# Performance work log

Measured on AMD Instinct MI355X. Metric: run time of the kernel, lower is better.

## Reference

```python
import jax, jax.numpy as jnp
import numpy as np

H = 1024
B = 8
S = 2048

def setup_inputs() -> dict:
    key = jax.random.key(0)
    ks = jax.random.split(key, 16)
    w = lambda k, shp: (jax.random.normal(k, shp, dtype=jnp.float32) * 0.02)
    return {
        "hidden_states": jax.random.normal(ks[0], (B, S, H), dtype=jnp.float32),
        "context_vector": jax.random.normal(ks[1], (B, H), dtype=jnp.float32),
        # nn.Linear weights stored torch-style as [out, in]
        "Wq": w(ks[2], (H, H)), "bq": w(ks[3], (H,)),
        "Wk": w(ks[4], (H, H)), "bk": w(ks[5], (H,)),
        "Wv": w(ks[6], (H, H)), "bv": w(ks[7], (H,)),
        "Wcq": w(ks[8], (H, H)),  # only .weight.t() used in original (no bias)
        "Wck": w(ks[9], (H, H)),
        "g_qh": jax.random.normal(ks[10], (H, 1), dtype=jnp.float32),
        "g_kh": jax.random.normal(ks[11], (H, 1), dtype=jnp.float32),
        "g_qc": jax.random.normal(ks[12], (H, 1), dtype=jnp.float32),
        "g_kc": jax.random.normal(ks[13], (H, 1), dtype=jnp.float32),
    }

def reference(hidden_states, context_vector, Wq, bq, Wk, bk, Wv, bv, Wcq, Wck, g_qh, g_kh, g_qc, g_kc):
    # Linear projections (torch Linear: x @ W.T + b)
    query = jnp.einsum('bsh,oh->bso', hidden_states, Wq) + bq   # [B,S,H]
    key_  = jnp.einsum('bsh,oh->bso', hidden_states, Wk) + bk
    value = jnp.einsum('bsh,oh->bso', hidden_states, Wv) + bv

    # gate = sigmoid(Q @ g_h + (ctx @ g_c)[:,None,:])  -> [B,S,1]
    q_gate = jax.nn.sigmoid(query @ g_qh + (context_vector @ g_qc)[:, None, :])
    k_gate = jax.nn.sigmoid(key_  @ g_kh + (context_vector @ g_kc)[:, None, :])

    # context projections: ctx @ weight.t() (no bias in original usage) -> [B,1,H]
    ctx_q = (context_vector @ Wcq.T)[:, None, :]
    ctx_k = (context_vector @ Wck.T)[:, None, :]

    query_hat = (1.0 - q_gate) * query + q_gate * ctx_q
    key_hat   = (1.0 - k_gate) * key_  + k_gate * ctx_k

    scale = 1.0 / jnp.sqrt(jnp.asarray(H, dtype=jnp.float32))
    scores = jnp.einsum('bqh,bkh->bqk', query_hat, key_hat) * scale  # [B,S,S]
    probs = jax.nn.softmax(scores, axis=-1)
    output = jnp.einsum('bqk,bkh->bqh', probs, value)  # [B,S,H]
    return (output, scores)
```

## Files before the change

kernel.cpp:

```cpp
#include <hip/hip_runtime.h>
#include <cstdint>
#include <cstddef>

#define H 1024
#define NB 8
#define S 2048
#define MROWS (NB*S)

using short8  = __attribute__((ext_vector_type(8))) short;
using ushort8 = __attribute__((ext_vector_type(8))) unsigned short;
using f32x4   = __attribute__((ext_vector_type(4))) float;

__device__ __forceinline__ unsigned short f2bf(float f){
  union { float f; unsigned int u; } c; c.f = f;
  unsigned int u = c.u;
  return (unsigned short)((u + 0x7fffu + ((u >> 16) & 1u)) >> 16);
}
__device__ __forceinline__ float bf2f(unsigned short b){
  union { unsigned int u; float f; } c; c.u = ((unsigned int)b) << 16;
  return c.f;
}

__global__ __launch_bounds__(256) void k_prep(
    const float* __restrict__ Wq, const float* __restrict__ Wk, const float* __restrict__ Wv,
    const float* __restrict__ Wcq, const float* __restrict__ Wck, const float* __restrict__ ctx,
    const float* __restrict__ gqh, const float* __restrict__ gkh,
    const float* __restrict__ bq, const float* __restrict__ bk,
    const float* __restrict__ gqc, const float* __restrict__ gkc,
    unsigned short* __restrict__ wqb, unsigned short* __restrict__ wkb, unsigned short* __restrict__ wvb,
    float* __restrict__ up, float* __restrict__ ctxq, float* __restrict__ ctxk,
    float* __restrict__ scal)
{
  __shared__ float cs[NB * H];
  const int bid = blockIdx.x;
  const int t = threadIdx.x;
  if (bid < 3072){
    const int y = bid >> 10;
    const int x = bid & 1023;
    const float* src = y == 0 ? Wq : (y == 1 ? Wk : Wv);
    unsigned short* dst = y == 0 ? wqb : (y == 1 ? wkb : wvb);
    const int i = (x * 256 + t) * 4;
    float4 v = *reinterpret_cast<const float4*>(src + i);
    ushort4 o; o.x = f2bf(v.x); o.y = f2bf(v.y); o.z = f2bf(v.z); o.w = f2bf(v.w);
    *reinterpret_cast<ushort4*>(dst + i) = o;
  } else if (bid < 3136){
    const int sub = bid - 3072;
    const int z = sub >> 5;
    const int y = (sub >> 2) & 7;
    const int x = sub & 3;
    const float* W = z ? Wk : Wq;
    const float* g = z ? gkh : gqh;
    const int in = x * 256 + t;
    const int o0 = y * 128;
    float s = 0.f;
    for (int o = 0; o < 128; ++o) s = fmaf(W[(size_t)(o0 + o) * H + in], g[o0 + o], s);
    up[(z * 8 + y) * 1024 + in] = s;
  } else if (bid < 3648){
    const int sub = bid - 3136;
    const int y = sub >> 8;
    const int x = sub & 255;
    const float* W = y ? Wck : Wcq;
    float* out = y ? ctxk : ctxq;
    for (int i = t; i < NB * H; i += 256) cs[i] = ctx[i];
    __syncthreads();
    const int wid = t >> 6, lane = t & 63;
    const int row = x * 4 + wid;
    float a[NB];
    #pragma unroll
    for (int b = 0; b < NB; ++b) a[b] = 0.f;
    for (int i0 = 0; i0 < H; i0 += 64){
      const float w = W[(size_t)row * H + i0 + lane];
      #pragma unroll
      for (int b = 0; b < NB; ++b) a[b] = fmaf(w, cs[b * H + i0 + lane], a[b]);
    }
    #pragma unroll
    for (int b = 0; b < NB; ++b){
      float v = a[b];
      #pragma unroll
      for (int off = 32; off > 0; off >>= 1) v += __shfl_xor(v, off);
      if (lane == 0) out[b * H + row] = v;
    }
  } else {
    const int wid = t >> 6, lane = t & 63;
    for (int d = wid; d < 18; d += 4){
      const float *pa, *pb;
      if (d == 0){ pa = bq; pb = gqh; }
      else if (d == 1){ pa = bk; pb = gkh; }
      else if (d < 10){ pa = ctx + (d - 2) * H; pb = gqc; }
      else { pa = ctx + (d - 10) * H; pb = gkc; }
      float s = 0.f;
      for (int i = lane; i < H; i += 64) s = fmaf(pa[i], pb[i], s);
      #pragma unroll
      for (int off = 32; off > 0; off >>= 1) s += __shfl_xor(s, off);
      if (lane == 0) scal[d] = s;
    }
  }
}

__global__ void k_ucombine(const float* __restrict__ up, float* __restrict__ u2){
  int i = blockIdx.x * 256 + threadIdx.x;
  int z = i >> 10, h = i & 1023;
  float s = 0.f;
  #pragma unroll
  for (int c = 0; c < 8; ++c) s += up[(z * 8 + c) * 1024 + h];
  u2[i] = s;
}

__global__ __launch_bounds__(256) void k_prepass(const float* __restrict__ hs,
    const float* __restrict__ u2, const float* __restrict__ scal,
    unsigned short* __restrict__ hsb, float* __restrict__ gq, float* __restrict__ gk){
  const int t = threadIdx.x, wid = t >> 6, lane = t & 63;
  const int row = blockIdx.x * 4 + wid;
  const float* hrow = hs + (size_t)row * H;
  const float* u_q = u2;
  const float* u_k = u2 + 1024;
  unsigned short* orow = hsb + (size_t)row * H;
  float sq = 0.f, sk = 0.f;
  #pragma unroll
  for (int c = 0; c < 4; ++c){
    const int idx = (lane + c * 64) * 4;
    float4 v  = *reinterpret_cast<const float4*>(hrow + idx);
    float4 uq = *reinterpret_cast<const float4*>(u_q + idx);
    float4 uk = *reinterpret_cast<const float4*>(u_k + idx);
    ushort4 o; o.x = f2bf(v.x); o.y = f2bf(v.y); o.z = f2bf(v.z); o.w = f2bf(v.w);
    *reinterpret_cast<ushort4*>(orow + idx) = o;
    sq += v.x*uq.x + v.y*uq.y + v.z*uq.z + v.w*uq.w;
    sk += v.x*uk.x + v.y*uk.y + v.z*uk.z + v.w*uk.w;
  }
  #pragma unroll
  for (int off = 32; off > 0; off >>= 1){
    sq += __shfl_xor(sq, off);
    sk += __shfl_xor(sk, off);
  }
  if (lane == 0){
    const int b = row >> 11;
    gq[row] = 1.f / (1.f + __expf(-(sq + scal[0] + scal[2 + b])));
    gk[row] = 1.f / (1.f + __expf(-(sk + scal[1] + scal[10 + b])));
  }
}


#define VM0() do { asm volatile("s_waitcnt vmcnt(0)" ::: "memory"); } while(0)
#define BAR() do { asm volatile("" ::: "memory"); __builtin_amdgcn_s_barrier(); asm volatile("" ::: "memory"); } while(0)

template<int MODE>
__global__ __launch_bounds__(256, 3)
void k_gemm(const unsigned short* __restrict__ A, const unsigned short* __restrict__ B,
            int K, int ldA, int ldB, long long Abatch, long long Bbatch,
            const float* __restrict__ gq, const float* __restrict__ gk,
            const float* __restrict__ bq, const float* __restrict__ bk, const float* __restrict__ bv,
            const float* __restrict__ cq, const float* __restrict__ ck,
            unsigned short* __restrict__ oq, unsigned short* __restrict__ ok, unsigned short* __restrict__ ov,
            float* __restrict__ outf, long long outBatch, float scale, float* __restrict__ rsum)
{
  __shared__ __align__(16) short lds[20480];
  short* As = lds;
  short* Bs = lds + 8192;

  const int t = threadIdx.x;
  const int wid = t >> 6, lane = t & 63;
  const int wr = wid >> 1, wc = wid & 1;
  const int bz = blockIdx.z;
  const unsigned short* Ab = A + (size_t)bz * (size_t)Abatch;
  const unsigned short* Bb = B + (size_t)bz * (size_t)Bbatch;
  const int row0 = blockIdx.x * 128;
  const int col0 = blockIdx.y * 128;

  const unsigned short* srcA[4];
  const unsigned short* srcB[4];
  #pragma unroll
  for (int i = 0; i < 4; ++i){
    const int c = (wid*4 + i)*64 + lane;
    const int r = c >> 3, sl = c & 7;
    const int kcg = sl ^ (r & 7);
    srcA[i] = Ab + (size_t)(row0 + r) * (size_t)ldA + kcg*8;
    srcB[i] = Bb + (size_t)(col0 + r) * (size_t)ldB + kcg*8;
  }

  f32x4 acc[4][4] = {};
  short8 af[4], bf[4];

  const int nkt = K >> 6;
  for (int kt = 0; kt < nkt; ++kt){
    const int k0 = kt << 6;
    #pragma unroll
    for (int i = 0; i < 4; ++i){
      __builtin_amdgcn_global_load_lds(
        (const __attribute__((address_space(1))) void*)(srcA[i] + k0),
        (__attribute__((address_space(3))) void*)((char*)As + (wid*4 + i)*1024), 16, 0, 0);
      __builtin_amdgcn_global_load_lds(
        (const __attribute__((address_space(1))) void*)(srcB[i] + k0),
        (__attribute__((address_space(3))) void*)((char*)Bs + (wid*4 + i)*1024), 16, 0, 0);
    }
    VM0(); BAR();
    #pragma unroll
    for (int kk = 0; kk < 2; ++kk){
      #pragma unroll
      for (int m = 0; m < 4; ++m){
        const int ar = wr*64 + m*16 + (lane & 15);
        const int ssl = (kk*4 + (lane >> 4)) ^ (ar & 7);
        af[m] = *reinterpret_cast<const short8*>(&As[ar*64 + ssl*8]);
      }
      #pragma unroll
      for (int n = 0; n < 4; ++n){
        const int br = wc*64 + n*16 + (lane & 15);
        const int ssl = (kk*4 + (lane >> 4)) ^ (br & 7);
        bf[n] = *reinterpret_cast<const short8*>(&Bs[br*64 + ssl*8]);
      }
      __builtin_amdgcn_s_setprio(1);
      #pragma unroll
      for (int m = 0; m < 4; ++m)
        #pragma unroll
        for (int n = 0; n < 4; ++n)
          acc[m][n] = __builtin_amdgcn_mfma_f32_16x16x32_bf16(af[m], bf[n], acc[m][n], 0, 0, 0);
      __builtin_amdgcn_s_setprio(0);
    }
    BAR();
  }

  if constexpr (MODE == 0){
    const int which = col0 >> 10;
    const int lcol  = col0 & 1023;
    if (which < 2){
      const float* gate = which ? gk : gq;
      const float* bias = which ? bk : bq;
      const float* ctxv = which ? ck : cq;
      unsigned short* outb = which ? ok : oq;
      unsigned short* tp = (unsigned short*)lds;
      float* gl = (float*)((char*)lds + 34816);
      float* bl = gl + 128;
      float* cl = bl + 128;
      const int b = row0 >> 11;
      __syncthreads();
      if (t < 128){
        gl[t] = gate[row0 + t];
        bl[t] = bias[lcol + t];
        cl[t] = ctxv[b * H + lcol + t];
      }
      __syncthreads();
      #pragma unroll
      for (int m = 0; m < 4; ++m)
        #pragma unroll
        for (int r = 0; r < 4; ++r){
          const int lr = wr*64 + m*16 + (lane >> 4)*4 + r;
          const float g = gl[lr];
          #pragma unroll
          for (int n = 0; n < 4; ++n){
            const int lc = wc*64 + n*16 + (lane & 15);
            const float q = acc[m][n][r] + bl[lc];
            tp[lr*136 + lc] = f2bf((1.f - g) * q + g * cl[lc]);
          }
        }
      __syncthreads();
      const int rr = t & 127;
      const int cc = (t >> 7) * 64;
      const unsigned short* srcp = tp + rr*136 + cc;
      unsigned short* dst = outb + (size_t)(row0 + rr) * H + lcol + cc;
      #pragma unroll
      for (int i = 0; i < 64; i += 8)
        *reinterpret_cast<ushort8*>(dst + i) = *reinterpret_cast<const ushort8*>(srcp + i);
    } else {
      unsigned short* tp = (unsigned short*)lds;
      const int bb = row0 >> 11;
      const int s0 = row0 & (S - 1);
      __syncthreads();
      #pragma unroll
      for (int m = 0; m < 4; ++m)
        #pragma unroll
        for (int r = 0; r < 4; ++r){
          const int lr = wr*64 + m*16 + (lane >> 4)*4 + r;
          #pragma unroll
          for (int n = 0; n < 4; ++n){
            const int lc = wc*64 + n*16 + (lane & 15);
            tp[lc*136 + lr] = f2bf(acc[m][n][r] + bv[lcol + lc]);
          }
        }
      __syncthreads();
      const int hh = t & 127;
      const int sc = (t >> 7) * 64;
      const unsigned short* srcp = tp + hh*136 + sc;
      unsigned short* vout = ov + (size_t)bb * H * S + (size_t)(lcol + hh) * S + (size_t)(s0 + sc);
      #pragma unroll
      for (int i = 0; i < 64; i += 8)
        *reinterpret_cast<ushort8*>(vout + i) = *reinterpret_cast<const ushort8*>(srcp + i);
    }
  } else if constexpr (MODE == 3){
    float* rowacc = (float*)lds;
    __syncthreads();
    if (t < 128) rowacc[t] = 0.f;
    __syncthreads();
    #pragma unroll
    for (int m = 0; m < 4; ++m)
      #pragma unroll
      for (int r = 0; r < 4; ++r){
        const int lr = wr*64 + m*16 + (lane >> 4)*4 + r;
        const int grow = row0 + lr;
        float psum = 0.f;
        #pragma unroll
        for (int n = 0; n < 4; ++n){
          const int gcol = col0 + wc*64 + n*16 + (lane & 15);
          const float val = acc[m][n][r] * scale;
          outf[(size_t)bz * (size_t)outBatch + (size_t)grow * S + gcol] = val;
          const float pe = __expf(fminf(val, 80.f));
          const unsigned short pb = f2bf(pe);
          oq[(size_t)bz * (size_t)outBatch + (size_t)grow * S + gcol] = pb;
          psum += bf2f(pb);
        }
        #pragma unroll
        for (int off = 1; off < 16; off <<= 1) psum += __shfl_xor(psum, off);
        if ((lane & 15) == 0) atomicAdd(&rowacc[lr], psum);
      }
    __syncthreads();
    if (t < 128) atomicAdd(&rsum[bz * S + row0 + t], rowacc[t]);
  } else {
    float* rs = (float*)lds;
    __syncthreads();
    if (t < 128) rs[t] = 1.f / fmaxf(rsum[bz * S + row0 + t], 1e-35f);
    __syncthreads();
    #pragma unroll
    for (int m = 0; m < 4; ++m)
      #pragma unroll
      for (int r = 0; r < 4; ++r){
        const int lr = wr*64 + m*16 + (lane >> 4)*4 + r;
        const float inv = rs[lr];
        #pragma unroll
        for (int n = 0; n < 4; ++n){
          const int gcol = col0 + wc*64 + n*16 + (lane & 15);
          outf[(size_t)bz * (size_t)outBatch + (size_t)(row0 + lr) * H + gcol] = acc[m][n][r] * inv;
        }
      }
  }
}

extern "C" void kernel_launch(void* const* d_in, const int* in_sizes, int n_in,
                              void* d_out, int out_size, void* d_ws, size_t ws_size,
                              hipStream_t stream) {
  const float* hs  = (const float*)d_in[0];
  const float* ctx = (const float*)d_in[1];
  const float* Wq  = (const float*)d_in[2];
  const float* bq  = (const float*)d_in[3];
  const float* Wk  = (const float*)d_in[4];
  const float* bk  = (const float*)d_in[5];
  const float* Wv  = (const float*)d_in[6];
  const float* bv  = (const float*)d_in[7];
  const float* Wcq = (const float*)d_in[8];
  const float* Wck = (const float*)d_in[9];
  const float* gqh = (const float*)d_in[10];
  const float* gkh = (const float*)d_in[11];
  const float* gqc = (const float*)d_in[12];
  const float* gkc = (const float*)d_in[13];

  char* ws = (char*)d_ws;
  unsigned short* hsb   = (unsigned short*)(ws);
  unsigned short* qhat  = (unsigned short*)(ws + 33554432);
  unsigned short* khat  = (unsigned short*)(ws + 67108864);
  unsigned short* vt    = (unsigned short*)(ws + 100663296);
  unsigned short* probs = (unsigned short*)(ws + 134217728);
  unsigned short* wqb   = (unsigned short*)(ws + 201326592);
  unsigned short* wkb   = (unsigned short*)(ws + 203423744);
  unsigned short* wvb   = (unsigned short*)(ws + 205520896);
  float* up    = (float*)(ws + 207618048);
  float* u2    = (float*)(ws + 207683584);
  float* ctxq  = (float*)(ws + 207691776);
  float* ctxk  = (float*)(ws + 207724544);
  float* gq    = (float*)(ws + 207757312);
  float* gk    = (float*)(ws + 207822848);
  float* scal  = (float*)(ws + 207888384);
  float* rsum  = (float*)(ws + 207888640);

  float* out_attn   = (float*)d_out;
  float* out_scores = out_attn + (size_t)MROWS * H;

  hipMemsetAsync(rsum, 0, MROWS * sizeof(float), stream);

  k_prep<<<3649, 256, 0, stream>>>(Wq, Wk, Wv, Wcq, Wck, ctx, gqh, gkh, bq, bk, gqc, gkc,
      wqb, wkb, wvb, up, ctxq, ctxk, scal);
  k_ucombine<<<8, 256, 0, stream>>>(up, u2);
  k_prepass<<<MROWS / 4, 256, 0, stream>>>(hs, u2, scal, hsb, gq, gk);

  k_gemm<0><<<dim3(128, 24, 1), 256, 0, stream>>>(hsb, wqb, 1024, 1024, 1024, 0, 0,
      gq, gk, bq, bk, bv, ctxq, ctxk, qhat, khat, vt, nullptr, 0, 1.f, nullptr);

  k_gemm<3><<<dim3(16, 16, 8), 256, 0, stream>>>(qhat, khat, 1024, 1024, 1024,
      (long long)S * H, (long long)S * H,
      nullptr, nullptr, nullptr, nullptr, nullptr, nullptr, nullptr,
      probs, nullptr, nullptr, out_scores, (long long)S * S, 0.03125f, rsum);

  k_gemm<5><<<dim3(16, 8, 8), 256, 0, stream>>>(probs, vt, 2048, 2048, 2048,
      (long long)S * S, (long long)H * S,
      nullptr, nullptr, nullptr, nullptr, nullptr, nullptr, nullptr,
      nullptr, nullptr, nullptr, out_attn, (long long)S * H, 1.f, rsum);
}
```

Baseline: 343.8 us.

## Use 256x256 double-buffered pipelined GEMM for score and PV matmuls

The batched QK^T and PV GEMMs now run in a new 512-thread kernel with 256x256 tiles. It double-buffers LDS and interleaves global->LDS loads for the next k-tile with MFMA work, using partial vmcnt waits instead of a full wait before each tile. The projection GEMM keeps the old 128x128 kernel. The bigger tiles cut global traffic per FLOP and hide load latency, at the cost of 128 KB LDS, more registers, and fewer blocks (512 and 256), which may leave CUs underused.

```diff
diff --git a/kernel.cpp b/kernel.cpp
--- a/kernel.cpp
+++ b/kernel.cpp
@@ -139,19 +139,17 @@
   }
 }
 
-
+#define VM4() do { asm volatile("s_waitcnt vmcnt(4)" ::: "memory"); } while(0)
 #define VM0() do { asm volatile("s_waitcnt vmcnt(0)" ::: "memory"); } while(0)
 #define BAR() do { asm volatile("" ::: "memory"); __builtin_amdgcn_s_barrier(); asm volatile("" ::: "memory"); } while(0)
 
-template<int MODE>
 __global__ __launch_bounds__(256, 3)
-void k_gemm(const unsigned short* __restrict__ A, const unsigned short* __restrict__ B,
-            int K, int ldA, int ldB, long long Abatch, long long Bbatch,
+void k_gemm128(const unsigned short* __restrict__ A, const unsigned short* __restrict__ B,
+            int K, int ldA, int ldB,
             const float* __restrict__ gq, const float* __restrict__ gk,
             const float* __restrict__ bq, const float* __restrict__ bk, const float* __restrict__ bv,
             const float* __restrict__ cq, const float* __restrict__ ck,
-            unsigned short* __restrict__ oq, unsigned short* __restrict__ ok, unsigned short* __restrict__ ov,
-            float* __restrict__ outf, long long outBatch, float scale, float* __restrict__ rsum)
+            unsigned short* __restrict__ oq, unsigned short* __restrict__ ok, unsigned short* __restrict__ ov)
 {
   __shared__ __align__(16) short lds[20480];
   short* As = lds;
@@ -160,9 +158,6 @@
   const int t = threadIdx.x;
   const int wid = t >> 6, lane = t & 63;
   const int wr = wid >> 1, wc = wid & 1;
-  const int bz = blockIdx.z;
-  const unsigned short* Ab = A + (size_t)bz * (size_t)Abatch;
-  const unsigned short* Bb = B + (size_t)bz * (size_t)Bbatch;
   const int row0 = blockIdx.x * 128;
   const int col0 = blockIdx.y * 128;
 
@@ -173,8 +168,8 @@
     const int c = (wid*4 + i)*64 + lane;
     const int r = c >> 3, sl = c & 7;
     const int kcg = sl ^ (r & 7);
-    srcA[i] = Ab + (size_t)(row0 + r) * (size_t)ldA + kcg*8;
-    srcB[i] = Bb + (size_t)(col0 + r) * (size_t)ldB + kcg*8;
+    srcA[i] = A + (size_t)(row0 + r) * (size_t)ldA + kcg*8;
+    srcB[i] = B + (size_t)(col0 + r) * (size_t)ldB + kcg*8;
   }
 
   f32x4 acc[4][4] = {};
@@ -218,88 +213,164 @@
     BAR();
   }
 
-  if constexpr (MODE == 0){
-    const int which = col0 >> 10;
-    const int lcol  = col0 & 1023;
-    if (which < 2){
-      const float* gate = which ? gk : gq;
-      const float* bias = which ? bk : bq;
-      const float* ctxv = which ? ck : cq;
-      unsigned short* outb = which ? ok : oq;
-      unsigned short* tp = (unsigned short*)lds;
-      float* gl = (float*)((char*)lds + 34816);
-      float* bl = gl + 128;
-      float* cl = bl + 128;
-      const int b = row0 >> 11;
-      __syncthreads();
-      if (t < 128){
-        gl[t] = gate[row0 + t];
-        bl[t] = bias[lcol + t];
-        cl[t] = ctxv[b * H + lcol + t];
-      }
-      __syncthreads();
-      #pragma unroll
-      for (int m = 0; m < 4; ++m)
-        #pragma unroll
-        for (int r = 0; r < 4; ++r){
-          const int lr = wr*64 + m*16 + (lane >> 4)*4 + r;
-          const float g = gl[lr];
-          #pragma unroll
-          for (int n = 0; n < 4; ++n){
-            const int lc = wc*64 + n*16 + (lane & 15);
-            const float q = acc[m][n][r] + bl[lc];
-            tp[lr*136 + lc] = f2bf((1.f - g) * q + g * cl[lc]);
-          }
-        }
-      __syncthreads();
-      const int rr = t & 127;
-      const int cc = (t >> 7) * 64;
-      const unsigned short* srcp = tp + rr*136 + cc;
-      unsigned short* dst = outb + (size_t)(row0 + rr) * H + lcol + cc;
-      #pragma unroll
-      for (int i = 0; i < 64; i += 8)
-        *reinterpret_cast<ushort8*>(dst + i) = *reinterpret_cast<const ushort8*>(srcp + i);
-    } else {
-      unsigned short* tp = (unsigned short*)lds;
-      const int bb = row0 >> 11;
-      const int s0 = row0 & (S - 1);
-      __syncthreads();
-      #pragma unroll
-      for (int m = 0; m < 4; ++m)
-        #pragma unroll
-        for (int r = 0; r < 4; ++r){
-          const int lr = wr*64 + m*16 + (lane >> 4)*4 + r;
-          #pragma unroll
-          for (int n = 0; n < 4; ++n){
-            const int lc = wc*64 + n*16 + (lane & 15);
-            tp[lc*136 + lr] = f2bf(acc[m][n][r] + bv[lcol + lc]);
-          }
-        }
-      __syncthreads();
-      const int hh = t & 127;
-      const int sc = (t >> 7) * 64;
-      const unsigned short* srcp = tp + hh*136 + sc;
-      unsigned short* vout = ov + (size_t)bb * H * S + (size_t)(lcol + hh) * S + (size_t)(s0 + sc);
-      #pragma unroll
-      for (int i = 0; i < 64; i += 8)
-        *reinterpret_cast<ushort8*>(vout + i) = *reinterpret_cast<const ushort8*>(srcp + i);
-    }
-  } else if constexpr (MODE == 3){
-    float* rowacc = (float*)lds;
-    __syncthreads();
-    if (t < 128) rowacc[t] = 0.f;
+  const int which = col0 >> 10;
+  const int lcol  = col0 & 1023;
+  if (which < 2){
+    const float* gate = which ? gk : gq;
+    const float* bias = which ? bk : bq;
+    const float* ctxv = which ? ck : cq;
+    unsigned short* outb = which ? ok : oq;
+    unsigned short* tp = (unsigned short*)lds;
+    float* gl = (float*)((char*)lds + 34816);
+    float* bl = gl + 128;
+    float* cl = bl + 128;
+    const int b = row0 >> 11;
+    __syncthreads();
+    if (t < 128){
+      gl[t] = gate[row0 + t];
+      bl[t] = bias[lcol + t];
+      cl[t] = ctxv[b * H + lcol + t];
+    }
     __syncthreads();
     #pragma unroll
     for (int m = 0; m < 4; ++m)
       #pragma unroll
       for (int r = 0; r < 4; ++r){
         const int lr = wr*64 + m*16 + (lane >> 4)*4 + r;
+        const float g = gl[lr];
+        #pragma unroll
+        for (int n = 0; n < 4; ++n){
+          const int lc = wc*64 + n*16 + (lane & 15);
+          const float q = acc[m][n][r] + bl[lc];
+          tp[lr*136 + lc] = f2bf((1.f - g) * q + g * cl[lc]);
+        }
+      }
+    __syncthreads();
+    const int rr = t & 127;
+    const int cc = (t >> 7) * 64;
+    const unsigned short* srcp = tp + rr*136 + cc;
+    unsigned short* dst = outb + (size_t)(row0 + rr) * H + lcol + cc;
+    #pragma unroll
+    for (int i = 0; i < 64; i += 8)
+      *reinterpret_cast<ushort8*>(dst + i) = *reinterpret_cast<const ushort8*>(srcp + i);
+  } else {
+    unsigned short* tp = (unsigned short*)lds;
+    const int bb = row0 >> 11;
+    const int s0 = row0 & (S - 1);
+    __syncthreads();
+    #pragma unroll
+    for (int m = 0; m < 4; ++m)
+      #pragma unroll
+      for (int r = 0; r < 4; ++r){
+        const int lr = wr*64 + m*16 + (lane >> 4)*4 + r;
+        #pragma unroll
+        for (int n = 0; n < 4; ++n){
+          const int lc = wc*64 + n*16 + (lane & 15);
+          tp[lc*136 + lr] = f2bf(acc[m][n][r] + bv[lcol + lc]);
+        }
+      }
+    __syncthreads();
+    const int hh = t & 127;
+    const int sc = (t >> 7) * 64;
+    const unsigned short* srcp = tp + hh*136 + sc;
+    unsigned short* vout = ov + (size_t)bb * H * S + (size_t)(lcol + hh) * S + (size_t)(s0 + sc);
+    #pragma unroll
+    for (int i = 0; i < 64; i += 8)
+      *reinterpret_cast<ushort8*>(vout + i) = *reinterpret_cast<const ushort8*>(srcp + i);
+  }
+}
+
+
+#define STG(bufi, opi, halfi, koff, P0, P1) \
+  do { __builtin_amdgcn_global_load_lds((const __attribute__((address_space(1))) void*)(P0 + (koff)), \
+      (__attribute__((address_space(3))) void*)((char*)(&lds[bufi][opi][halfi][0]) + (wid*2+0)*1024), 16, 0, 0); \
+    __builtin_amdgcn_global_load_lds((const __attribute__((address_space(1))) void*)(P1 + (koff)), \
+      (__attribute__((address_space(3))) void*)((char*)(&lds[bufi][opi][halfi][0]) + (wid*2+1)*1024), 16, 0, 0); } while(0)
+#define STG_A(bufi, halfi, koff) STG(bufi, 0, halfi, koff, sA0, sA1)
+#define STG_B(bufi, halfi, koff) STG(bufi, 1, halfi, koff, sB0, sB1)
+
+#define DS_A(bufi, ks, mh) \
+  do { _Pragma("unroll") for (int m_ = 0; m_ < 4; ++m_){ \
+      const int ar_ = wr*128 + ((mh)*4 + m_)*16 + (lane & 15); \
+      const int sl_ = (lane >> 4) ^ ((ar_ >> 1) & 3); \
+      af[m_] = *reinterpret_cast<const short8*>(&lds[bufi][0][ks][ar_*32 + sl_*8]); } } while(0)
+#define DS_B(bufi, ks) \
+  do { _Pragma("unroll") for (int n_ = 0; n_ < 4; ++n_){ \
+      const int br_ = wc*64 + n_*16 + (lane & 15); \
+      const int sl_ = (lane >> 4) ^ ((br_ >> 1) & 3); \
+      bf[n_] = *reinterpret_cast<const short8*>(&lds[bufi][1][ks][br_*32 + sl_*8]); } } while(0)
+#define MFMA16(mh) \
+  do { __builtin_amdgcn_s_setprio(1); \
+    _Pragma("unroll") for (int m_ = 0; m_ < 4; ++m_) \
+      _Pragma("unroll") for (int n_ = 0; n_ < 4; ++n_) \
+        acc[(mh)*4 + m_][n_] = __builtin_amdgcn_mfma_f32_16x16x32_bf16(af[m_], bf[n_], acc[(mh)*4 + m_][n_], 0, 0, 0); \
+    __builtin_amdgcn_s_setprio(0); } while(0)
+
+template<int MODE>
+__global__ __launch_bounds__(512, 2)
+void k_gemm256(const unsigned short* __restrict__ A, const unsigned short* __restrict__ B,
+            int K, int ldA, int ldB, long long Abatch, long long Bbatch,
+            unsigned short* __restrict__ oq,
+            float* __restrict__ outf, long long outBatch, float scale, float* __restrict__ rsum)
+{
+  __shared__ __align__(16) short lds[2][2][2][8192];
+
+  const int t = threadIdx.x;
+  const int wid = t >> 6, lane = t & 63;
+  const int wr = wid >> 2, wc = wid & 3;
+  const int bz = blockIdx.z;
+  const unsigned short* Ab = A + (size_t)bz * (size_t)Abatch;
+  const unsigned short* Bb = B + (size_t)bz * (size_t)Bbatch;
+  const int row0 = blockIdx.x * 256;
+  const int col0 = blockIdx.y * 256;
+
+  const int c0 = (wid*2 + 0)*64 + lane;
+  const int c1 = (wid*2 + 1)*64 + lane;
+  const int r0s = c0 >> 2, r1s = c1 >> 2;
+  const int kc0 = (c0 & 3) ^ ((r0s >> 1) & 3);
+  const int kc1 = (c1 & 3) ^ ((r1s >> 1) & 3);
+  const unsigned short* sA0 = Ab + (size_t)(row0 + r0s) * (size_t)ldA + kc0*8;
+  const unsigned short* sA1 = Ab + (size_t)(row0 + r1s) * (size_t)ldA + kc1*8;
+  const unsigned short* sB0 = Bb + (size_t)(col0 + r0s) * (size_t)ldB + kc0*8;
+  const unsigned short* sB1 = Bb + (size_t)(col0 + r1s) * (size_t)ldB + kc1*8;
+
+  f32x4 acc[8][4] = {};
+  short8 af[4], bf[4];
+
+  STG_A(0, 0, 0); STG_B(0, 0, 0); STG_A(0, 1, 32); STG_B(0, 1, 32);
+  VM0(); BAR();
+
+  const int niter = K >> 7;
+  for (int it = 0; it < niter; ++it){
+    const int t1k = (it*2 + 1) << 6;
+    const int t2k = (it*2 + 2) << 6;
+    const bool more = (it + 1 < niter);
+    DS_A(0, 0, 0); DS_B(0, 0); STG_A(1, 0, t1k);      MFMA16(0);                              BAR();
+    DS_A(0, 0, 1);             STG_B(1, 0, t1k);      MFMA16(1); VM4();                       BAR();
+    DS_A(0, 1, 0); DS_B(0, 1); STG_A(1, 1, t1k + 32); MFMA16(0);                              BAR();
+    DS_A(0, 1, 1);             STG_B(1, 1, t1k + 32); MFMA16(1); if (more) { VM4(); } else { VM0(); } BAR();
+    DS_A(1, 0, 0); DS_B(1, 0); if (more) { STG_A(0, 0, t2k); }      MFMA16(0);                BAR();
+    DS_A(1, 0, 1);             if (more) { STG_B(0, 0, t2k); }      MFMA16(1); if (more) { VM4(); } BAR();
+    DS_A(1, 1, 0); DS_B(1, 1); if (more) { STG_A(0, 1, t2k + 32); } MFMA16(0);                BAR();
+    DS_A(1, 1, 1);             if (more) { STG_B(0, 1, t2k + 32); } MFMA16(1); if (more) { VM4(); } BAR();
+  }
+
+  if constexpr (MODE == 3){
+    float* rowacc = (float*)lds;
+    __syncthreads();
+    if (t < 256) rowacc[t] = 0.f;
+    __syncthreads();
+    #pragma unroll
+    for (int mi = 0; mi < 8; ++mi)
+      #pragma unroll
+      for (int r = 0; r < 4; ++r){
+        const int lr = wr*128 + mi*16 + (lane >> 4)*4 + r;
         const int grow = row0 + lr;
         float psum = 0.f;
         #pragma unroll
         for (int n = 0; n < 4; ++n){
           const int gcol = col0 + wc*64 + n*16 + (lane & 15);
-          const float val = acc[m][n][r] * scale;
+          const float val = acc[mi][n][r] * scale;
           outf[(size_t)bz * (size_t)outBatch + (size_t)grow * S + gcol] = val;
           const float pe = __expf(fminf(val, 80.f));
           const unsigned short pb = f2bf(pe);
@@ -311,22 +382,22 @@
         if ((lane & 15) == 0) atomicAdd(&rowacc[lr], psum);
       }
     __syncthreads();
-    if (t < 128) atomicAdd(&rsum[bz * S + row0 + t], rowacc[t]);
+    if (t < 256) atomicAdd(&rsum[bz * S + row0 + t], rowacc[t]);
   } else {
     float* rs = (float*)lds;
     __syncthreads();
-    if (t < 128) rs[t] = 1.f / fmaxf(rsum[bz * S + row0 + t], 1e-35f);
-    __syncthreads();
-    #pragma unroll
-    for (int m = 0; m < 4; ++m)
+    if (t < 256) rs[t] = 1.f / fmaxf(rsum[bz * S + row0 + t], 1e-35f);
+    __syncthreads();
+    #pragma unroll
+    for (int mi = 0; mi < 8; ++mi)
       #pragma unroll
       for (int r = 0; r < 4; ++r){
-        const int lr = wr*64 + m*16 + (lane >> 4)*4 + r;
+        const int lr = wr*128 + mi*16 + (lane >> 4)*4 + r;
         const float inv = rs[lr];
         #pragma unroll
         for (int n = 0; n < 4; ++n){
           const int gcol = col0 + wc*64 + n*16 + (lane & 15);
-          outf[(size_t)bz * (size_t)outBatch + (size_t)(row0 + lr) * H + gcol] = acc[m][n][r] * inv;
+          outf[(size_t)bz * (size_t)outBatch + (size_t)(row0 + lr) * H + gcol] = acc[mi][n][r] * inv;
         }
       }
   }
@@ -378,16 +449,14 @@
   k_ucombine<<<8, 256, 0, stream>>>(up, u2);
   k_prepass<<<MROWS / 4, 256, 0, stream>>>(hs, u2, scal, hsb, gq, gk);
 
-  k_gemm<0><<<dim3(128, 24, 1), 256, 0, stream>>>(hsb, wqb, 1024, 1024, 1024, 0, 0,
-      gq, gk, bq, bk, bv, ctxq, ctxk, qhat, khat, vt, nullptr, 0, 1.f, nullptr);
-
-  k_gemm<3><<<dim3(16, 16, 8), 256, 0, stream>>>(qhat, khat, 1024, 1024, 1024,
+  k_gemm128<<<dim3(128, 24, 1), 256, 0, stream>>>(hsb, wqb, 1024, 1024, 1024,
+      gq, gk, bq, bk, bv, ctxq, ctxk, qhat, khat, vt);
+
+  k_gemm256<3><<<dim3(8, 8, 8), 512, 0, stream>>>(qhat, khat, 1024, 1024, 1024,
       (long long)S * H, (long long)S * H,
-      nullptr, nullptr, nullptr, nullptr, nullptr, nullptr, nullptr,
-      probs, nullptr, nullptr, out_scores, (long long)S * S, 0.03125f, rsum);
-
-  k_gemm<5><<<dim3(16, 8, 8), 256, 0, stream>>>(probs, vt, 2048, 2048, 2048,
+      probs, out_scores, (long long)S * S, 0.03125f, rsum);
+
+  k_gemm256<5><<<dim3(8, 4, 8), 512, 0, stream>>>(probs, vt, 2048, 2048, 2048,
       (long long)S * S, (long long)H * S,
-      nullptr, nullptr, nullptr, nullptr, nullptr, nullptr, nullptr,
-      nullptr, nullptr, nullptr, out_attn, (long long)S * H, 1.f, rsum);
-}
+      nullptr, out_attn, (long long)S * H, 1.f, rsum);
+}
```

Measured after the change: 322.6 us. 6.2% less time.
